# Kernel optimization log

Measured on AMD Instinct MI355X. Metric: run time of the kernel, lower is better.

## Reference

```python
import jax, jax.numpy as jnp
import numpy as np
from jax import lax

B, L, D, H = 32, 512, 1024, 1024


def setup_inputs() -> dict:
    key = jax.random.key(0)
    kx, kw, kb = jax.random.split(key, 3)
    x = jax.random.normal(kx, (B, L, D), dtype=jnp.float32)
    # nn.Linear(D+H, 4H): weight (4H, D+H), bias (4H,), uniform(-1/sqrt(fan_in), 1/sqrt(fan_in))
    bound = 1.0 / np.sqrt(D + H)
    W = jax.random.uniform(kw, (4 * H, D + H), minval=-bound, maxval=bound, dtype=jnp.float32)
    b = jax.random.uniform(kb, (4 * H,), minval=-bound, maxval=bound, dtype=jnp.float32)
    return {"x": x, "W": W, "b": b}


def reference(x, W, b):
    Bsz, Lseq, Din = x.shape
    Hd = W.shape[0] // 4

    def step(carry, x_t):
        h, c = carry
        combined = jnp.concatenate([h, x_t], axis=-1)          # (B, H+D)
        gates = combined @ W.T + b                              # (B, 4H)
        f, i, o, c_tilde = jnp.split(gates, 4, axis=-1)
        c_new = jax.nn.sigmoid(f) * c + jax.nn.sigmoid(i) * jnp.tanh(c_tilde)
        h_new = jax.nn.sigmoid(o) * jnp.tanh(c_new)
        return (h_new, c_new), h_new

    h0 = jnp.zeros((Bsz, Hd), dtype=x.dtype)
    c0 = jnp.zeros((Bsz, Hd), dtype=x.dtype)
    xs = jnp.transpose(x, (1, 0, 2))                            # (L, B, D)
    _, hs = lax.scan(step, (h0, c0), xs)                        # hs: (L, B, H)
    return jnp.transpose(hs, (1, 0, 2))                         # (B, L, H)
```

## Files before the change

### kernel.cpp

```cpp
#include <hip/hip_runtime.h>
#include <hip/hip_fp16.h>

#define B_SZ 32
#define L_SZ 512
#define D_SZ 1024
#define H_SZ 1024
#define NG   4096
#define M_SZ 16384

typedef __attribute__((ext_vector_type(8))) short short8;
typedef __attribute__((ext_vector_type(4))) float f32x4;
typedef __attribute__((ext_vector_type(4))) unsigned u32x4;
typedef __attribute__((ext_vector_type(4))) unsigned short u16x4;

static const size_t GX_OFF  = 0;
static const size_t XB_OFF  = 134217728;
static const size_t WH_OFF  = 167772160;
static const size_t WX_OFF  = 176160768;
static const size_t FLG_OFF = 184680448;

__device__ __forceinline__ unsigned short f2bf(float f) {
  union { float f; unsigned u; } v; v.f = f;
  unsigned r = v.u + 0x7fffu + ((v.u >> 16) & 1u);
  return (unsigned short)(r >> 16);
}

__device__ __forceinline__ void gload_lds16(const void* g, void* l) {
  __builtin_amdgcn_global_load_lds(
      (const __attribute__((address_space(1))) unsigned*)g,
      (__attribute__((address_space(3))) unsigned*)l, 16, 0, 0);
}


__global__ __launch_bounds__(256) void k_convert_w(const float* __restrict__ W,
                                                   unsigned short* __restrict__ Wh,
                                                   unsigned short* __restrict__ Wx) {
  int idx = blockIdx.x * 256 + threadIdx.x;
  f32x4 v = ((const f32x4*)W)[idx];
  u16x4 o;
#pragma unroll
  for (int e = 0; e < 4; ++e) o[e] = f2bf(v[e]);
  int n   = idx >> 9;
  int col = (idx & 511) * 4;
  if (col < 1024) *(u16x4*)(Wh + (size_t)n * 1024 + col)          = o;
  else            *(u16x4*)(Wx + (size_t)n * 1024 + (col - 1024)) = o;
}

__global__ __launch_bounds__(256) void k_convert_x(const float* __restrict__ x,
                                                   unsigned short* __restrict__ xb) {
  int idx = blockIdx.x * 256 + threadIdx.x;
  f32x4 v = ((const f32x4*)x)[idx];
  u16x4 o;
#pragma unroll
  for (int e = 0; e < 4; ++e) o[e] = f2bf(v[e]);
  unsigned long long val;
  __builtin_memcpy(&val, &o, 8);
  unsigned short* p = xb + (size_t)idx * 4;
  asm volatile("global_store_dwordx2 %0, %1, off sc0 sc1"
               :: "v"(p), "v"(val) : "memory");
}

__global__ __launch_bounds__(256) void k_zero_wt(unsigned* __restrict__ p, int n) {
  int i = blockIdx.x * 256 + threadIdx.x;
  unsigned z = 0u;
  if (i < n)
    asm volatile("global_store_dword %0, %1, off sc0 sc1"
                 :: "v"(p + i), "v"(z) : "memory");
}


__global__ __launch_bounds__(256) void k_xgemm(const unsigned short* __restrict__ A,
                                               const unsigned short* __restrict__ Bw,
                                               __half* __restrict__ C) {
  __shared__ unsigned short sA[128 * 64];
  __shared__ unsigned short sB[128 * 64];
  const int m0 = blockIdx.x * 128;
  const int n0 = blockIdx.y * 128;
  const int tid = threadIdx.x;
  const int lane = tid & 63;
  const int w = tid >> 6;
  const int wm = w >> 1, wn = w & 1;
  f32x4 acc[4][4] = {};
  for (int k0 = 0; k0 < 1024; k0 += 64) {
#pragma unroll
    for (int it = 0; it < 4; ++it) {
      int chunk = it * 256 + w * 64 + lane;
      int row = chunk >> 3, kc = chunk & 7;
      gload_lds16(A + (size_t)(m0 + row) * 1024 + k0 + kc * 8,
                  (char*)sA + (size_t)(it * 256 + w * 64) * 16);
      gload_lds16(Bw + (size_t)(n0 + row) * 1024 + k0 + kc * 8,
                  (char*)sB + (size_t)(it * 256 + w * 64) * 16);
    }
    asm volatile("s_waitcnt vmcnt(0)" ::: "memory");
    __syncthreads();
#pragma unroll
    for (int ks = 0; ks < 2; ++ks) {
      short8 af[4], bfr[4];
#pragma unroll
      for (int i = 0; i < 4; ++i) {
        int arow = wm * 64 + i * 16 + (lane & 15);
        af[i] = *(const short8*)(sA + arow * 64 + ks * 32 + (lane >> 4) * 8);
      }
#pragma unroll
      for (int j = 0; j < 4; ++j) {
        int brow = wn * 64 + j * 16 + (lane & 15);
        bfr[j] = *(const short8*)(sB + brow * 64 + ks * 32 + (lane >> 4) * 8);
      }
#pragma unroll
      for (int i = 0; i < 4; ++i)
#pragma unroll
        for (int j = 0; j < 4; ++j)
          acc[i][j] = __builtin_amdgcn_mfma_f32_16x16x32_bf16(af[i], bfr[j], acc[i][j], 0, 0, 0);
    }
    __syncthreads();
  }
#pragma unroll
  for (int i = 0; i < 4; ++i)
#pragma unroll
    for (int j = 0; j < 4; ++j)
#pragma unroll
      for (int q = 0; q < 4; ++q) {
        int row = m0 + wm * 64 + i * 16 + (lane >> 4) * 4 + q;
        int col = n0 + wn * 64 + j * 16 + (lane & 15);
        C[(size_t)row * NG + col] = __float2half(acc[i][j][q]);
      }
}


__global__ __launch_bounds__(256, 1) void k_lstm(const unsigned short* __restrict__ Whg,
                                                 const __half* __restrict__ Gx,
                                                 const float* __restrict__ bias,
                                                 unsigned short* __restrict__ ring,
                                                 float* __restrict__ out,
                                                 unsigned* __restrict__ flags) {
  extern __shared__ char lds[];
  char* h_base  = lds;
  float* part   = (float*)(lds + 65536);
  float* bias_s = (float*)(lds + 65536 + 18432);
  unsigned short* hlds = (unsigned short*)(lds + 65536 + 18432 + 128);

  const int tid = threadIdx.x;
  const int lane = tid & 63;
  const int wv = tid >> 6;
  const int wg = blockIdx.x;
  const int j0 = wg * 8;

  __builtin_amdgcn_fence(__ATOMIC_ACQUIRE, "agent");

  short8 bfrag[2][8];
#pragma unroll
  for (int ntx = 0; ntx < 2; ++ntx) {
#pragma unroll
    for (int ks = 0; ks < 8; ++ks) {
      int br = ntx * 16 + (lane & 15);
      const unsigned short* src = Whg
          + (size_t)((br >> 3) * 1024 + j0 + (br & 7)) * 1024
          + wv * 256 + ks * 32 + (lane >> 4) * 8;
      bfrag[ntx][ks] = *(const short8*)src;
    }
  }
  if (tid < 32) bias_s[tid] = bias[(tid >> 3) * 1024 + j0 + (tid & 7)];
  __syncthreads();

  const int row0 = lane & 15;
  const char* aB0 = h_base + row0 * 2048;
  const char* aB1 = h_base + (16 + row0) * 2048;
  const int kslot = (lane >> 4) * 16;
  const int aswz = (row0 & 7) << 4;
  const int kbyte0 = wv * 512;
  const int b_ = tid >> 3, jj = tid & 7;
  const float rb0 = bias_s[jj], rb1 = bias_s[8 + jj];
  const float rb2 = bias_s[16 + jj], rb3 = bias_s[24 + jj];
  float c_reg = 0.f;

  const unsigned* fp0 = flags + (size_t)(2 * tid) * 16;
  const unsigned* fp1 = flags + (size_t)(2 * tid + 1) * 16;

  for (int t = 0; t < 512; ++t) {
    const char* hin = (const char*)ring + (size_t)t * 65536;
    unsigned short* hout = ring + (size_t)(t + 1) * 32768;

    u32x4 hz = {0u, 0u, 0u, 0u};
    u32x4 h0=hz,h1=hz,h2=hz,h3=hz,h4=hz,h5=hz,h6=hz,h7=hz,
          h8=hz,h9=hz,h10=hz,h11=hz,h12=hz,h13=hz,h14=hz,h15=hz;
    if (t) {
#define HLD(r, it) asm volatile("global_load_dwordx4 %0, %1, off" \
      : "=v"(r) : "v"(hin + (size_t)((it) * 256 + tid) * 16) : "memory")
      HLD(h0,0); HLD(h1,1); HLD(h2,2); HLD(h3,3);
      HLD(h4,4); HLD(h5,5); HLD(h6,6); HLD(h7,7);
      HLD(h8,8); HLD(h9,9); HLD(h10,10); HLD(h11,11);
      HLD(h12,12); HLD(h13,13); HLD(h14,14); HLD(h15,15);
#undef HLD
    }
    const char* gxp = (const char*)(Gx + ((size_t)(b_ * L_SZ + t)) * NG + j0 + jj);
    unsigned gxa, gxb, gxc, gxd;
    asm volatile("global_load_ushort %0, %1, off" : "=v"(gxa) : "v"(gxp)        : "memory");
    asm volatile("global_load_ushort %0, %1, off" : "=v"(gxb) : "v"(gxp + 2048) : "memory");
    asm volatile("global_load_ushort %0, %1, off" : "=v"(gxc) : "v"(gxp + 4096) : "memory");
    asm volatile("global_load_ushort %0, %1, off" : "=v"(gxd) : "v"(gxp + 6144) : "memory");

#define HWR(r, it) { int i_ = (it) * 256 + tid; int bb_ = i_ >> 7, kc_ = i_ & 127; \
      *(u32x4*)(h_base + bb_ * 2048 + ((kc_ * 16) ^ ((bb_ & 7) << 4))) = r; }
    asm volatile("s_waitcnt vmcnt(12)" ::: "memory");
    __builtin_amdgcn_sched_barrier(0);
    HWR(h0,0); HWR(h1,1); HWR(h2,2); HWR(h3,3);
    HWR(h4,4); HWR(h5,5); HWR(h6,6); HWR(h7,7);
    asm volatile("s_waitcnt vmcnt(4)" ::: "memory");
    __builtin_amdgcn_sched_barrier(0);
    HWR(h8,8); HWR(h9,9); HWR(h10,10); HWR(h11,11);
    HWR(h12,12); HWR(h13,13); HWR(h14,14); HWR(h15,15);
#undef HWR
    __syncthreads();

    f32x4 acc00 = {0.f,0.f,0.f,0.f}, acc01 = {0.f,0.f,0.f,0.f};
    f32x4 acc10 = {0.f,0.f,0.f,0.f}, acc11 = {0.f,0.f,0.f,0.f};
#pragma unroll
    for (int ks = 0; ks < 8; ++ks) {
      int kb = kbyte0 + ks * 64 + kslot;
      short8 a0 = *(const short8*)(aB0 + (kb ^ aswz));
      short8 a1 = *(const short8*)(aB1 + (kb ^ aswz));
      acc00 = __builtin_amdgcn_mfma_f32_16x16x32_bf16(a0, bfrag[0][ks], acc00, 0, 0, 0);
      acc01 = __builtin_amdgcn_mfma_f32_16x16x32_bf16(a0, bfrag[1][ks], acc01, 0, 0, 0);
      acc10 = __builtin_amdgcn_mfma_f32_16x16x32_bf16(a1, bfrag[0][ks], acc10, 0, 0, 0);
      acc11 = __builtin_amdgcn_mfma_f32_16x16x32_bf16(a1, bfrag[1][ks], acc11, 0, 0, 0);
    }
    {
      float* pw = part + wv * 1152;
      int r0 = (lane >> 4) * 4, cA = lane & 15;
#pragma unroll
      for (int q = 0; q < 4; ++q) {
        pw[(r0 + q) * 36 + cA]           = acc00[q];
        pw[(r0 + q) * 36 + 16 + cA]      = acc01[q];
        pw[(16 + r0 + q) * 36 + cA]      = acc10[q];
        pw[(16 + r0 + q) * 36 + 16 + cA] = acc11[q];
      }
    }
    __syncthreads();

    float s0 = 0.f, s1 = 0.f, s2 = 0.f, s3 = 0.f;
#pragma unroll
    for (int p = 0; p < 4; ++p) {
      const float* pp = part + p * 1152 + b_ * 36 + jj;
      s0 += pp[0]; s1 += pp[8]; s2 += pp[16]; s3 += pp[24];
    }
    asm volatile("s_waitcnt vmcnt(0)" ::: "memory");
    __builtin_amdgcn_sched_barrier(0);
    float hn;
    {
      float sf = s0 + __half2float(__ushort_as_half((unsigned short)gxa)) + rb0;
      float si = s1 + __half2float(__ushort_as_half((unsigned short)gxb)) + rb1;
      float so = s2 + __half2float(__ushort_as_half((unsigned short)gxc)) + rb2;
      float sc = s3 + __half2float(__ushort_as_half((unsigned short)gxd)) + rb3;
      float gf = 1.f / (1.f + expf(-sf));
      float gi = 1.f / (1.f + expf(-si));
      float go = 1.f / (1.f + expf(-so));
      float cn = gf * c_reg + gi * tanhf(sc);
      hn = go * tanhf(cn);
      c_reg = cn;
      hlds[tid] = f2bf(hn);
    }
    float* outp = out + ((size_t)b_ * L_SZ + t) * H_SZ + j0 + jj;

    if (t < 511) {
      __syncthreads();
      if (tid < 32) {
        u32x4 v = *(u32x4*)(hlds + tid * 8);
        unsigned short* hp = hout + (size_t)tid * H_SZ + j0;
        asm volatile("global_store_dwordx4 %0, %1, off sc0 sc1"
                     :: "v"(hp), "v"(v) : "memory");
      }
      asm volatile("s_waitcnt vmcnt(0)" ::: "memory");
      if (tid == 0) {
        unsigned fv = (unsigned)(t + 1);
        const unsigned* myf = flags + (size_t)wg * 16;
        asm volatile("global_store_dword %0, %1, off sc0 sc1"
                     :: "v"(myf), "v"(fv) : "memory");
      }
      *outp = hn;
      if (tid < 64) {
        unsigned fa, fb;
        do {
          asm volatile("global_load_dword %0, %2, off sc0 sc1\n\t"
                       "global_load_dword %1, %3, off sc0 sc1\n\t"
                       "s_waitcnt vmcnt(0)"
                       : "=v"(fa), "=v"(fb) : "v"(fp0), "v"(fp1) : "memory");
        } while (!__all(fa > (unsigned)t && fb > (unsigned)t));
      }
      __syncthreads();
    } else {
      *outp = hn;
    }
  }
}


extern "C" void kernel_launch(void* const* d_in, const int* in_sizes, int n_in,
                              void* d_out, int out_size, void* d_ws, size_t ws_size,
                              hipStream_t stream) {
  const float* x = (const float*)d_in[0];
  const float* W = (const float*)d_in[1];
  const float* b = (const float*)d_in[2];
  char* ws = (char*)d_ws;
  __half* Gx           = (__half*)(ws + GX_OFF);
  unsigned short* xb   = (unsigned short*)(ws + XB_OFF);
  unsigned short* Wh   = (unsigned short*)(ws + WH_OFF);
  unsigned short* Wx   = (unsigned short*)(ws + WX_OFF);
  unsigned* flags      = (unsigned*)(ws + FLG_OFF);
  float* out = (float*)d_out;

  k_convert_w<<<8192, 256, 0, stream>>>(W, Wh, Wx);
  k_convert_x<<<16384, 256, 0, stream>>>(x, xb);
  k_zero_wt<<<8, 256, 0, stream>>>(flags, 8192 / 4);

  k_xgemm<<<dim3(128, 32), 256, 0, stream>>>(xb, Wx, Gx);

  (void)hipFuncSetAttribute((const void*)k_lstm,
                            hipFuncAttributeMaxDynamicSharedMemorySize, 84608);
  k_lstm<<<128, 256, 84608, stream>>>(Wh, Gx, b, xb, out, flags);
}
```

Measured before the change: 2.163 ms.

## Load recurrent h fragments directly into registers and use fast gate math

Each wave now loads its MFMA A-fragments of the previous hidden state straight from global memory into registers. This replaces staging the full h tile in swizzled LDS, which removes a block-wide barrier and LDS traffic per timestep and shrinks dynamic shared memory. Sigmoid and tanh switch to __expf-based fast versions with clamping. The trade-off is that each wave rereads overlapping h rows from global or cache, with some accuracy loss in the activations.

```diff
diff --git a/kernel.cpp b/kernel.cpp
--- a/kernel.cpp
+++ b/kernel.cpp
@@ -23,6 +23,13 @@
   union { float f; unsigned u; } v; v.f = f;
   unsigned r = v.u + 0x7fffu + ((v.u >> 16) & 1u);
   return (unsigned short)(r >> 16);
+}
+
+__device__ __forceinline__ float fsig(float x) { return 1.f / (1.f + __expf(-x)); }
+__device__ __forceinline__ float ftanh(float x) {
+  x = fminf(fmaxf(x, -15.f), 15.f);
+  float e = __expf(-2.f * x);
+  return (1.f - e) / (1.f + e);
 }
 
 __device__ __forceinline__ void gload_lds16(const void* g, void* l) {
@@ -134,10 +141,9 @@
                                                  float* __restrict__ out,
                                                  unsigned* __restrict__ flags) {
   extern __shared__ char lds[];
-  char* h_base  = lds;
-  float* part   = (float*)(lds + 65536);
-  float* bias_s = (float*)(lds + 65536 + 18432);
-  unsigned short* hlds = (unsigned short*)(lds + 65536 + 18432 + 128);
+  float* part   = (float*)lds;
+  float* bias_s = (float*)(lds + 18432);
+  unsigned short* hlds = (unsigned short*)(lds + 18432 + 128);
 
   const int tid = threadIdx.x;
   const int lane = tid & 63;
@@ -162,12 +168,8 @@
   if (tid < 32) bias_s[tid] = bias[(tid >> 3) * 1024 + j0 + (tid & 7)];
   __syncthreads();
 
-  const int row0 = lane & 15;
-  const char* aB0 = h_base + row0 * 2048;
-  const char* aB1 = h_base + (16 + row0) * 2048;
-  const int kslot = (lane >> 4) * 16;
-  const int aswz = (row0 & 7) << 4;
-  const int kbyte0 = wv * 512;
+  const size_t aoff0 = (size_t)(lane & 15) * 2048 + (size_t)wv * 512 + (size_t)(lane >> 4) * 16;
+  const size_t aoff1 = aoff0 + 16 * 2048;
   const int b_ = tid >> 3, jj = tid & 7;
   const float rb0 = bias_s[jj], rb1 = bias_s[8 + jj];
   const float rb2 = bias_s[16 + jj], rb3 = bias_s[24 + jj];
@@ -180,18 +182,6 @@
     const char* hin = (const char*)ring + (size_t)t * 65536;
     unsigned short* hout = ring + (size_t)(t + 1) * 32768;
 
-    u32x4 hz = {0u, 0u, 0u, 0u};
-    u32x4 h0=hz,h1=hz,h2=hz,h3=hz,h4=hz,h5=hz,h6=hz,h7=hz,
-          h8=hz,h9=hz,h10=hz,h11=hz,h12=hz,h13=hz,h14=hz,h15=hz;
-    if (t) {
-#define HLD(r, it) asm volatile("global_load_dwordx4 %0, %1, off" \
-      : "=v"(r) : "v"(hin + (size_t)((it) * 256 + tid) * 16) : "memory")
-      HLD(h0,0); HLD(h1,1); HLD(h2,2); HLD(h3,3);
-      HLD(h4,4); HLD(h5,5); HLD(h6,6); HLD(h7,7);
-      HLD(h8,8); HLD(h9,9); HLD(h10,10); HLD(h11,11);
-      HLD(h12,12); HLD(h13,13); HLD(h14,14); HLD(h15,15);
-#undef HLD
-    }
     const char* gxp = (const char*)(Gx + ((size_t)(b_ * L_SZ + t)) * NG + j0 + jj);
     unsigned gxa, gxb, gxc, gxd;
     asm volatile("global_load_ushort %0, %1, off" : "=v"(gxa) : "v"(gxp)        : "memory");
@@ -199,26 +189,34 @@
     asm volatile("global_load_ushort %0, %1, off" : "=v"(gxc) : "v"(gxp + 4096) : "memory");
     asm volatile("global_load_ushort %0, %1, off" : "=v"(gxd) : "v"(gxp + 6144) : "memory");
 
-#define HWR(r, it) { int i_ = (it) * 256 + tid; int bb_ = i_ >> 7, kc_ = i_ & 127; \
-      *(u32x4*)(h_base + bb_ * 2048 + ((kc_ * 16) ^ ((bb_ & 7) << 4))) = r; }
-    asm volatile("s_waitcnt vmcnt(12)" ::: "memory");
+    u32x4 a0r[8], a1r[8];
+    if (t) {
+      const char* aG0 = hin + aoff0;
+      const char* aG1 = hin + aoff1;
+#pragma unroll
+      for (int ks = 0; ks < 8; ++ks) {
+        asm volatile("global_load_dwordx4 %0, %1, off offset:%2"
+                     : "=v"(a0r[ks]) : "v"(aG0), "n"(ks * 64) : "memory");
+        asm volatile("global_load_dwordx4 %0, %1, off offset:%2"
+                     : "=v"(a1r[ks]) : "v"(aG1), "n"(ks * 64) : "memory");
+      }
+    } else {
+#pragma unroll
+      for (int ks = 0; ks < 8; ++ks) {
+        a0r[ks] = (u32x4){0u, 0u, 0u, 0u};
+        a1r[ks] = (u32x4){0u, 0u, 0u, 0u};
+      }
+    }
+    asm volatile("s_waitcnt vmcnt(0)" ::: "memory");
     __builtin_amdgcn_sched_barrier(0);
-    HWR(h0,0); HWR(h1,1); HWR(h2,2); HWR(h3,3);
-    HWR(h4,4); HWR(h5,5); HWR(h6,6); HWR(h7,7);
-    asm volatile("s_waitcnt vmcnt(4)" ::: "memory");
-    __builtin_amdgcn_sched_barrier(0);
-    HWR(h8,8); HWR(h9,9); HWR(h10,10); HWR(h11,11);
-    HWR(h12,12); HWR(h13,13); HWR(h14,14); HWR(h15,15);
-#undef HWR
-    __syncthreads();
 
     f32x4 acc00 = {0.f,0.f,0.f,0.f}, acc01 = {0.f,0.f,0.f,0.f};
     f32x4 acc10 = {0.f,0.f,0.f,0.f}, acc11 = {0.f,0.f,0.f,0.f};
 #pragma unroll
     for (int ks = 0; ks < 8; ++ks) {
-      int kb = kbyte0 + ks * 64 + kslot;
-      short8 a0 = *(const short8*)(aB0 + (kb ^ aswz));
-      short8 a1 = *(const short8*)(aB1 + (kb ^ aswz));
+      short8 a0, a1;
+      __builtin_memcpy(&a0, &a0r[ks], 16);
+      __builtin_memcpy(&a1, &a1r[ks], 16);
       acc00 = __builtin_amdgcn_mfma_f32_16x16x32_bf16(a0, bfrag[0][ks], acc00, 0, 0, 0);
       acc01 = __builtin_amdgcn_mfma_f32_16x16x32_bf16(a0, bfrag[1][ks], acc01, 0, 0, 0);
       acc10 = __builtin_amdgcn_mfma_f32_16x16x32_bf16(a1, bfrag[0][ks], acc10, 0, 0, 0);
@@ -243,19 +241,14 @@
       const float* pp = part + p * 1152 + b_ * 36 + jj;
       s0 += pp[0]; s1 += pp[8]; s2 += pp[16]; s3 += pp[24];
     }
-    asm volatile("s_waitcnt vmcnt(0)" ::: "memory");
-    __builtin_amdgcn_sched_barrier(0);
     float hn;
     {
       float sf = s0 + __half2float(__ushort_as_half((unsigned short)gxa)) + rb0;
       float si = s1 + __half2float(__ushort_as_half((unsigned short)gxb)) + rb1;
       float so = s2 + __half2float(__ushort_as_half((unsigned short)gxc)) + rb2;
       float sc = s3 + __half2float(__ushort_as_half((unsigned short)gxd)) + rb3;
-      float gf = 1.f / (1.f + expf(-sf));
-      float gi = 1.f / (1.f + expf(-si));
-      float go = 1.f / (1.f + expf(-so));
-      float cn = gf * c_reg + gi * tanhf(sc);
-      hn = go * tanhf(cn);
+      float cn = fsig(sf) * c_reg + fsig(si) * ftanh(sc);
+      hn = fsig(so) * ftanh(cn);
       c_reg = cn;
       hlds[tid] = f2bf(hn);
     }
@@ -314,7 +307,5 @@
 
   k_xgemm<<<dim3(128, 32), 256, 0, stream>>>(xb, Wx, Gx);
 
-  (void)hipFuncSetAttribute((const void*)k_lstm,
-                            hipFuncAttributeMaxDynamicSharedMemorySize, 84608);
-  k_lstm<<<128, 256, 84608, stream>>>(Wh, Gx, b, xb, out, flags);
-}
+  k_lstm<<<128, 256, 19072, stream>>>(Wh, Gx, b, xb, out, flags);
+}
```

New measurement: 2.715 ms. 1.26x slower.
